# Kernel optimization log

Hardware: AMD Instinct MI355X
Metric: run time of the kernel (lower is better)

## Reference

```python
import jax, jax.numpy as jnp
import numpy as np

N_QUBITS = 12
DIM = 2 ** N_QUBITS
BATCH = 2048


def setup_inputs() -> dict:
    key = jax.random.key(0)
    k1, k2, k3 = jax.random.split(key, 3)
    inputs = jax.random.normal(k1, (BATCH, N_QUBITS), dtype=jnp.float32)
    weight = jax.random.normal(k2, (3 + 2 * N_QUBITS,), dtype=jnp.float32)
    entangle_matrix = jax.random.normal(k3, (DIM, DIM), dtype=jnp.float32)
    return {"inputs": inputs, "weight": weight, "entangle_matrix": entangle_matrix}


def _encode(ry_angles, rz_angles):
    # Encoder: state = prod over qubits of first column of (Rz*Ry) per qubit.
    ry = ry_angles / 2
    rz = rz_angles / 2
    a = jnp.cos(ry) * jnp.exp(-1j * rz)  # entry11 (row bit = 0)
    b = jnp.sin(ry) * jnp.exp(1j * rz)   # entry21 (row bit = 1)
    col2 = jnp.stack([a, b], axis=-1).astype(jnp.complex64)  # [B, n, 2]
    B, n = ry.shape
    v = jnp.ones((B, 1), dtype=jnp.complex64)
    for q in range(n):  # Kronecker fold over qubits (big-endian, matches dec2bin)
        v = (v[:, :, None] * col2[:, q][:, None, :]).reshape(B, -1)
    return v  # [B, 2^n]


def _rot_mat(w):
    # rot_mat: per-qubit Rx(w[q]) @ Rz(w[n+q]), then full Kronecker product.
    n = w.shape[0] // 2
    tx = (w[:n] / 2).astype(jnp.complex64)
    tz = (w[n:] / 2).astype(jnp.complex64)
    c, s = jnp.cos(tx), jnp.sin(tx)
    rx = jnp.stack([jnp.stack([c, -1j * s], -1),
                    jnp.stack([-1j * s, c], -1)], -2)  # [n,2,2]
    ez = jnp.exp(-1j * tz)
    zero = jnp.zeros_like(ez)
    rz = jnp.stack([jnp.stack([ez, zero], -1),
                    jnp.stack([zero, jnp.exp(1j * tz)], -1)], -2)  # [n,2,2]
    mats = jnp.einsum('qij,qjk->qik', rx, rz)
    M = mats[0]
    for q in range(1, n):
        M = jnp.kron(M, mats[q])
    return M  # [2^n, 2^n]


def _ry2(theta):
    a = theta / 2
    c, s = jnp.cos(a), jnp.sin(a)
    return jnp.stack([jnp.stack([c, -s]), jnp.stack([s, c])])  # [2,2] real


def _final_rot(th3):
    # final_rot_mat: Rz-form @ Ry-form @ Rx-form (all ry_mat_list), kron with identity.
    rot = _ry2(th3[2]) @ (_ry2(th3[1]) @ _ry2(th3[0]))
    eye = jnp.eye(DIM // 2, dtype=jnp.complex64)
    return jnp.kron(rot.astype(jnp.complex64), eye)  # [DIM, DIM]


def reference(inputs, weight, entangle_matrix):
    # initial=False branch
    ry_angles = inputs
    rz_angles = jnp.square(inputs)
    v = _encode(ry_angles, rz_angles)                 # [B, DIM] complex64
    E = entangle_matrix.astype(jnp.complex64)
    R = _rot_mat(weight[3:])
    M = E @ R @ E                                     # [DIM, DIM]
    v = v @ M.T                                       # tensordot dims ([-1],[-1])
    F = _final_rot(weight[:3])
    v = v @ F.T
    half = DIM // 2
    # vector[:, half:] = 0 then sum |.|^2  <=>  sum over first half
    return jnp.sum(jnp.square(jnp.abs(v[:, :half])), axis=-1)  # [B] float32
```

## Files before the change

kernel.cpp:

```cpp
#include <hip/hip_runtime.h>
#include <math.h>

#define QDIM 4096
#define NQ 12
#define QBATCH 2048

typedef _Float16 f16x8 __attribute__((ext_vector_type(8)));
typedef float f32x4 __attribute__((ext_vector_type(4)));
typedef int i32x4 __attribute__((ext_vector_type(4)));

__device__ __forceinline__ void gld_lds16(const void* gptr, void* ldsptr) {
    __builtin_amdgcn_global_load_lds(
        (const __attribute__((address_space(1))) void*)gptr,
        (__attribute__((address_space(3))) void*)ldsptr,
        16, 0, 0);
}

__device__ __forceinline__ int q8(float x) {
    float y = fminf(fmaxf(x, -127.f), 127.f);
    return (int)rintf(y);
}
__device__ __forceinline__ int pack4_i8(int a, int b, int c, int d) {
    return (a & 0xFF) | ((b & 0xFF) << 8) | ((c & 0xFF) << 16) | ((d & 0xFF) << 24);
}

__global__ __launch_bounds__(256) void conv_kernel(
    const float* __restrict__ E, const float* __restrict__ wgt,
    _Float16* __restrict__ Eh, signed char* __restrict__ G8)
{
    float th = 0.5f * (wgt[0] + wgt[1] + wgt[2]);
    float c0 = cosf(th), c1 = -sinf(th);
    const float qs = 127.f / 6.f;
    size_t flat = ((size_t)blockIdx.x * 256 + threadIdx.x) * 8;
    size_t n = flat >> 12;
    size_t k = flat & (QDIM - 1);
    const float* p0 = E + n * QDIM + k;
    const float* p1 = p0 + (size_t)QBATCH * QDIM;
    float4 a0 = ((const float4*)p0)[0], a1 = ((const float4*)p0)[1];
    float4 b0 = ((const float4*)p1)[0], b1 = ((const float4*)p1)[1];
    f16x8 h0 = { (_Float16)a0.x, (_Float16)a0.y, (_Float16)a0.z, (_Float16)a0.w,
                 (_Float16)a1.x, (_Float16)a1.y, (_Float16)a1.z, (_Float16)a1.w };
    f16x8 h1 = { (_Float16)b0.x, (_Float16)b0.y, (_Float16)b0.z, (_Float16)b0.w,
                 (_Float16)b1.x, (_Float16)b1.y, (_Float16)b1.z, (_Float16)b1.w };
    *(f16x8*)&Eh[n * QDIM + k] = h0;
    *(f16x8*)&Eh[(n + QBATCH) * QDIM + k] = h1;
    float g[8] = { c0*a0.x + c1*b0.x, c0*a0.y + c1*b0.y, c0*a0.z + c1*b0.z, c0*a0.w + c1*b0.w,
                   c0*a1.x + c1*b1.x, c0*a1.y + c1*b1.y, c0*a1.z + c1*b1.z, c0*a1.w + c1*b1.w };
    int2 gp = { pack4_i8(q8(g[0]*qs), q8(g[1]*qs), q8(g[2]*qs), q8(g[3]*qs)),
                pack4_i8(q8(g[4]*qs), q8(g[5]*qs), q8(g[6]*qs), q8(g[7]*qs)) };
    *(int2*)&G8[n * QDIM + k] = gp;
}

__global__ __launch_bounds__(256) void expand_kernel(
    const float* __restrict__ inputs, _Float16* __restrict__ A1)
{
    __shared__ float ab[NQ][4];
    const int b = blockIdx.x;
    const int tid = threadIdx.x;
    if (tid < NQ) {
        float x = inputs[b * NQ + tid];
        float ry = 0.5f * x;
        float rz = 0.5f * x * x;
        float ca = cosf(ry), sa = sinf(ry), cz = cosf(rz), sz = sinf(rz);
        ab[tid][0] = ca * cz;  ab[tid][1] = -ca * sz;
        ab[tid][2] = sa * cz;  ab[tid][3] =  sa * sz;
    }
    __syncthreads();
    float pr0 = 1.f, pi0 = 0.f;
#pragma unroll
    for (int q = 0; q < 8; ++q) {
        int bit = (tid >> (7 - q)) & 1;
        float cr = ab[q][bit * 2 + 0], ci = ab[q][bit * 2 + 1];
        float nr = pr0 * cr - pi0 * ci;
        float ni = pr0 * ci + pi0 * cr;
        pr0 = nr; pi0 = ni;
    }
    f16x8 vr[2], vi[2];
#pragma unroll
    for (int u = 0; u < 16; ++u) {
        float pr = pr0, pi = pi0;
#pragma unroll
        for (int q = 8; q < 12; ++q) {
            int bit = (u >> (11 - q)) & 1;
            float cr = ab[q][bit * 2 + 0], ci = ab[q][bit * 2 + 1];
            float nr = pr * cr - pi * ci;
            float ni = pr * ci + pi * cr;
            pr = nr; pi = ni;
        }
        vr[u >> 3][u & 7] = (_Float16)pr;
        vi[u >> 3][u & 7] = (_Float16)pi;
    }
    const int idx0 = tid * 16;
    *(f16x8*)&A1[(size_t)b * QDIM + idx0] = vr[0];
    *(f16x8*)&A1[(size_t)b * QDIM + idx0 + 8] = vr[1];
    *(f16x8*)&A1[(size_t)(b + QBATCH) * QDIM + idx0] = vi[0];
    *(f16x8*)&A1[(size_t)(b + QBATCH) * QDIM + idx0 + 8] = vi[1];
}

__global__ __launch_bounds__(256) void gemm_f16(
    const _Float16* __restrict__ A, const _Float16* __restrict__ B,
    _Float16* __restrict__ C, int N)
{
    const int K = QDIM;
    __shared__ __attribute__((aligned(16))) _Float16 As[128 * 64];
    __shared__ __attribute__((aligned(16))) _Float16 Bs[128 * 64];

    const int tid  = threadIdx.x;
    const int wave = tid >> 6;
    const int lane = tid & 63;
    const int bn0 = blockIdx.x * 128;
    const int bm0 = blockIdx.y * 128;
    const int wm = (wave >> 1) * 64;
    const int wn = (wave & 1) * 64;
    const int q = lane >> 4;
    const int r = lane & 15;
    const int rx = r & 7;

    f32x4 acc[4][4];
#pragma unroll
    for (int i = 0; i < 4; ++i)
#pragma unroll
        for (int j = 0; j < 4; ++j) acc[i][j] = (f32x4){0.f, 0.f, 0.f, 0.f};

    const _Float16* gA[4];
    const _Float16* gB[4];
    char* lA[4];
    char* lB[4];
#pragma unroll
    for (int n = 0; n < 4; ++n) {
        int c = n * 256 + tid;
        int row = c >> 3;
        int gcol = (c & 7) ^ (row & 7);
        gA[n] = A + (size_t)(bm0 + row) * K + gcol * 8;
        gB[n] = B + (size_t)(bn0 + row) * K + gcol * 8;
        lA[n] = (char*)As + (n * 256 + wave * 64) * 16;
        lB[n] = (char*)Bs + (n * 256 + wave * 64) * 16;
    }

    for (int kk = 0; kk < K; kk += 64) {
#pragma unroll
        for (int n = 0; n < 4; ++n) {
            gld_lds16(gA[n] + kk, lA[n]);
            gld_lds16(gB[n] + kk, lB[n]);
        }
        __syncthreads();

#pragma unroll
        for (int s = 0; s < 2; ++s) {
            f16x8 af[4], bf[4];
#pragma unroll
            for (int i = 0; i < 4; ++i) {
                int row = wm + i * 16 + r;
                af[i] = *(const f16x8*)&As[(row * 8 + ((s * 4 + q) ^ rx)) * 8];
            }
#pragma unroll
            for (int j = 0; j < 4; ++j) {
                int row = wn + j * 16 + r;
                bf[j] = *(const f16x8*)&Bs[(row * 8 + ((s * 4 + q) ^ rx)) * 8];
            }
#pragma unroll
            for (int i = 0; i < 4; ++i)
#pragma unroll
                for (int j = 0; j < 4; ++j)
                    acc[i][j] = __builtin_amdgcn_mfma_f32_16x16x32_f16(af[i], bf[j], acc[i][j], 0, 0, 0);
        }
        __syncthreads();
    }

#pragma unroll
    for (int i = 0; i < 4; ++i) {
        const int crow = bm0 + wm + i * 16 + q * 4;
#pragma unroll
        for (int rr = 0; rr < 4; ++rr)
#pragma unroll
            for (int j = 0; j < 4; ++j)
                C[(size_t)(crow + rr) * N + bn0 + wn + j * 16 + r] = (_Float16)acc[i][j][rr];
    }
}

__global__ __launch_bounds__(256) void butterfly_kernel(
    const _Float16* __restrict__ u1, const float* __restrict__ wgt,
    signed char* __restrict__ A2, float* __restrict__ scaleA)
{
    __shared__ float sRe[QDIM];
    __shared__ float sIm[QDIM];
    __shared__ float mats[NQ][8];
    __shared__ float red[8];
    const int b = blockIdx.x;
    const int tid = threadIdx.x;

    if (tid < NQ) {
        float tx = 0.5f * wgt[3 + tid];
        float tz = 0.5f * wgt[15 + tid];
        float c = cosf(tx), s = sinf(tx), cz = cosf(tz), sz = sinf(tz);
        mats[tid][0] =  c * cz;  mats[tid][1] = -c * sz;
        mats[tid][2] =  s * sz;  mats[tid][3] = -s * cz;
        mats[tid][4] = -s * sz;  mats[tid][5] = -s * cz;
        mats[tid][6] =  c * cz;  mats[tid][7] =  c * sz;
    }
    const int base = tid * 16;
    const _Float16* pRe = u1 + (size_t)b * QDIM + base;
    const _Float16* pIm = u1 + (size_t)(b + QBATCH) * QDIM + base;
    float xr[16], xi[16];
    {
        f16x8 r0 = ((const f16x8*)pRe)[0], r1 = ((const f16x8*)pRe)[1];
        f16x8 i0 = ((const f16x8*)pIm)[0], i1 = ((const f16x8*)pIm)[1];
#pragma unroll
        for (int j = 0; j < 8; ++j) {
            xr[j] = (float)r0[j]; xr[8 + j] = (float)r1[j];
            xi[j] = (float)i0[j]; xi[8 + j] = (float)i1[j];
        }
    }
    __syncthreads();

#pragma unroll
    for (int p = 0; p < 4; ++p) {
        const int qq = 11 - p;
        const float m00r = mats[qq][0], m00i = mats[qq][1];
        const float m01r = mats[qq][2], m01i = mats[qq][3];
        const float m10r = mats[qq][4], m10i = mats[qq][5];
        const float m11r = mats[qq][6], m11i = mats[qq][7];
#pragma unroll
        for (int t = 0; t < 8; ++t) {
            int i0 = ((t >> p) << (p + 1)) | (t & ((1 << p) - 1));
            int i1 = i0 | (1 << p);
            float x0r = xr[i0], x0i = xi[i0];
            float x1r = xr[i1], x1i = xi[i1];
            xr[i0] = m00r * x0r - m00i * x0i + m01r * x1r - m01i * x1i;
            xi[i0] = m00r * x0i + m00i * x0r + m01r * x1i + m01i * x1r;
            xr[i1] = m10r * x0r - m10i * x0i + m11r * x1r - m11i * x1i;
            xi[i1] = m10r * x0i + m10i * x0r + m11r * x1i + m11i * x1r;
        }
    }
#pragma unroll
    for (int j = 0; j < 16; ++j) { sRe[base + j] = xr[j]; sIm[base + j] = xi[j]; }
    __syncthreads();

    for (int p = 4; p < 12; ++p) {
        const int qq = 11 - p;
        const float m00r = mats[qq][0], m00i = mats[qq][1];
        const float m01r = mats[qq][2], m01i = mats[qq][3];
        const float m10r = mats[qq][4], m10i = mats[qq][5];
        const float m11r = mats[qq][6], m11i = mats[qq][7];
        for (int t = tid; t < QDIM / 2; t += 256) {
            int i0 = ((t >> p) << (p + 1)) | (t & ((1 << p) - 1));
            int i1 = i0 | (1 << p);
            float x0r = sRe[i0], x0i = sIm[i0];
            float x1r = sRe[i1], x1i = sIm[i1];
            sRe[i0] = m00r * x0r - m00i * x0i + m01r * x1r - m01i * x1i;
            sIm[i0] = m00r * x0i + m00i * x0r + m01r * x1i + m01i * x1r;
            sRe[i1] = m10r * x0r - m10i * x0i + m11r * x1r - m11i * x1i;
            sIm[i1] = m10r * x0i + m10i * x0r + m11r * x1i + m11i * x1r;
        }
        __syncthreads();
    }

    float mR = 0.f, mI = 0.f;
#pragma unroll
    for (int j = 0; j < 16; ++j) {
        mR = fmaxf(mR, fabsf(sRe[base + j]));
        mI = fmaxf(mI, fabsf(sIm[base + j]));
    }
#pragma unroll
    for (int off = 32; off > 0; off >>= 1) {
        mR = fmaxf(mR, __shfl_xor(mR, off, 64));
        mI = fmaxf(mI, __shfl_xor(mI, off, 64));
    }
    const int wid = tid >> 6;
    if ((tid & 63) == 0) { red[wid] = mR; red[4 + wid] = mI; }
    __syncthreads();
    mR = fmaxf(fmaxf(red[0], red[1]), fmaxf(red[2], red[3]));
    mI = fmaxf(fmaxf(red[4], red[5]), fmaxf(red[6], red[7]));
    mR = fmaxf(mR, 1e-30f);
    mI = fmaxf(mI, 1e-30f);
    if (tid == 0) {
        scaleA[b] = mR / 127.f;
        scaleA[b + QBATCH] = mI / 127.f;
    }
    const float invR = 127.f / mR, invI = 127.f / mI;
    i32x4 qr, qi;
#pragma unroll
    for (int w = 0; w < 4; ++w) {
        qr[w] = pack4_i8(q8(sRe[base + 4*w] * invR), q8(sRe[base + 4*w + 1] * invR),
                         q8(sRe[base + 4*w + 2] * invR), q8(sRe[base + 4*w + 3] * invR));
        qi[w] = pack4_i8(q8(sIm[base + 4*w] * invI), q8(sIm[base + 4*w + 1] * invI),
                         q8(sIm[base + 4*w + 2] * invI), q8(sIm[base + 4*w + 3] * invI));
    }
    *(i32x4*)&A2[(size_t)b * QDIM + base] = qr;
    *(i32x4*)&A2[(size_t)(b + QBATCH) * QDIM + base] = qi;
}

__global__ __launch_bounds__(256) void gemm2_i8(
    const signed char* __restrict__ A, const signed char* __restrict__ B,
    const float* __restrict__ scaleA, float* __restrict__ out)
{
    const int K = QDIM;
    __shared__ __attribute__((aligned(16))) signed char As[128 * 128];
    __shared__ __attribute__((aligned(16))) signed char Bs[128 * 128];

    const int tid  = threadIdx.x;
    const int wave = tid >> 6;
    const int lane = tid & 63;
    const int bn0 = blockIdx.x * 128;
    const int bm0 = blockIdx.y * 128;
    const int wm = (wave >> 1) * 64;
    const int wn = (wave & 1) * 64;
    const int q = lane >> 4;
    const int r = lane & 15;
    const int rx = r & 7;

    i32x4 acc[4][4];
#pragma unroll
    for (int i = 0; i < 4; ++i)
#pragma unroll
        for (int j = 0; j < 4; ++j) acc[i][j] = (i32x4){0, 0, 0, 0};

    const signed char* gA[4];
    const signed char* gB[4];
    char* lA[4];
    char* lB[4];
#pragma unroll
    for (int n = 0; n < 4; ++n) {
        int c = n * 256 + tid;
        int row = c >> 3;
        int gcol = (c & 7) ^ (row & 7);
        gA[n] = A + (size_t)(bm0 + row) * K + gcol * 16;
        gB[n] = B + (size_t)(bn0 + row) * K + gcol * 16;
        lA[n] = (char*)As + (n * 256 + wave * 64) * 16;
        lB[n] = (char*)Bs + (n * 256 + wave * 64) * 16;
    }

    for (int kk = 0; kk < K; kk += 128) {
#pragma unroll
        for (int n = 0; n < 4; ++n) {
            gld_lds16(gA[n] + kk, lA[n]);
            gld_lds16(gB[n] + kk, lB[n]);
        }
        __syncthreads();

#pragma unroll
        for (int s = 0; s < 2; ++s) {
            i32x4 af[4], bf[4];
#pragma unroll
            for (int i = 0; i < 4; ++i) {
                int row = wm + i * 16 + r;
                af[i] = *(const i32x4*)&As[row * 128 + (((s * 4 + q) ^ rx) * 16)];
            }
#pragma unroll
            for (int j = 0; j < 4; ++j) {
                int row = wn + j * 16 + r;
                bf[j] = *(const i32x4*)&Bs[row * 128 + (((s * 4 + q) ^ rx) * 16)];
            }
#pragma unroll
            for (int i = 0; i < 4; ++i)
#pragma unroll
                for (int j = 0; j < 4; ++j)
                    acc[i][j] = __builtin_amdgcn_mfma_i32_16x16x64_i8(af[i], bf[j], acc[i][j], 0, 0, 0);
        }
        __syncthreads();
    }

    const float dqG = 6.f / 127.f;
#pragma unroll
    for (int i = 0; i < 4; ++i) {
#pragma unroll
        for (int rr = 0; rr < 4; ++rr) {
            const int row = bm0 + wm + i * 16 + q * 4 + rr;
            const float sc = scaleA[row] * dqG;
            float v = 0.f;
#pragma unroll
            for (int j = 0; j < 4; ++j) {
                float t = sc * (float)acc[i][j][rr];
                v = fmaf(t, t, v);
            }
            v += __shfl_xor(v, 1, 64);
            v += __shfl_xor(v, 2, 64);
            v += __shfl_xor(v, 4, 64);
            v += __shfl_xor(v, 8, 64);
            if (r == 0) atomicAdd(&out[row & (QBATCH - 1)], v);
        }
    }
}

__global__ __launch_bounds__(256) void zero_out(float* __restrict__ out) {
    ((float4*)out)[blockIdx.x * 256 + threadIdx.x] = (float4){0.f, 0.f, 0.f, 0.f};
}

extern "C" void kernel_launch(void* const* d_in, const int* in_sizes, int n_in,
                              void* d_out, int out_size, void* d_ws, size_t ws_size,
                              hipStream_t stream)
{
    const float* inputs = (const float*)d_in[0];
    const float* weight = (const float*)d_in[1];
    const float* E      = (const float*)d_in[2];
    float* out = (float*)d_out;

    char* ws = (char*)d_ws;
    const size_t MB = 1024 * 1024;
    _Float16*    Eh     = (_Float16*)   (ws + 0);
    signed char* G8     = (signed char*)(ws + 32 * MB);
    _Float16*    A1     = (_Float16*)   (ws + 40 * MB);
    _Float16*    u1     = (_Float16*)   (ws + 72 * MB);
    signed char* A2     = (signed char*)(ws + 104 * MB);
    float*       scaleA = (float*)      (ws + 120 * MB);

    conv_kernel<<<(QBATCH * QDIM / 8) / 256, 256, 0, stream>>>(E, weight, Eh, G8);
    expand_kernel<<<QBATCH, 256, 0, stream>>>(inputs, A1);
    gemm_f16<<<dim3(QDIM / 128, QDIM / 128), 256, 0, stream>>>(A1, Eh, u1, QDIM);
    butterfly_kernel<<<QBATCH, 256, 0, stream>>>(u1, weight, A2, scaleA);
    zero_out<<<QBATCH / 1024, 256, 0, stream>>>(out);
    gemm2_i8<<<dim3(2048 / 128, QDIM / 128), 256, 0, stream>>>(A2, G8, scaleA, out);
}
```

Measured before the change: 336.7 us.

## Restructure butterfly as three register-resident radix-16 passes with padded LDS transposes

Replaces the eight shared-memory butterfly stages, each ending in a barrier, with three passes of four in-register stages. Data moves between passes through padded shared-memory transposes (strides 273 and 17) meant to avoid bank conflicts. This cuts LDS traffic and barriers. The zero_out launch is removed by zeroing the output inside expand_kernel. In exchange, the final int8 stores become strided single-byte writes instead of 16-byte vector stores.

```diff
diff --git a/kernel.cpp b/kernel.cpp
--- a/kernel.cpp
+++ b/kernel.cpp
@@ -52,11 +52,13 @@
 }
 
 __global__ __launch_bounds__(256) void expand_kernel(
-    const float* __restrict__ inputs, _Float16* __restrict__ A1)
+    const float* __restrict__ inputs, _Float16* __restrict__ A1,
+    float* __restrict__ out)
 {
     __shared__ float ab[NQ][4];
     const int b = blockIdx.x;
     const int tid = threadIdx.x;
+    if (tid == 0) out[b] = 0.f;
     if (tid < NQ) {
         float x = inputs[b * NQ + tid];
         float ry = 0.5f * x;
@@ -182,12 +184,14 @@
     const _Float16* __restrict__ u1, const float* __restrict__ wgt,
     signed char* __restrict__ A2, float* __restrict__ scaleA)
 {
-    __shared__ float sRe[QDIM];
-    __shared__ float sIm[QDIM];
+    __shared__ float sRe[4366];
+    __shared__ float sIm[4366];
     __shared__ float mats[NQ][8];
     __shared__ float red[8];
-    const int b = blockIdx.x;
+    const int blk = blockIdx.x;
     const int tid = threadIdx.x;
+    const int ah = tid >> 4;
+    const int al = tid & 15;
 
     if (tid < NQ) {
         float tx = 0.5f * wgt[3 + tid];
@@ -198,11 +202,11 @@
         mats[tid][4] = -s * sz;  mats[tid][5] = -s * cz;
         mats[tid][6] =  c * cz;  mats[tid][7] =  c * sz;
     }
-    const int base = tid * 16;
-    const _Float16* pRe = u1 + (size_t)b * QDIM + base;
-    const _Float16* pIm = u1 + (size_t)(b + QBATCH) * QDIM + base;
+
     float xr[16], xi[16];
     {
+        const _Float16* pRe = u1 + (size_t)blk * QDIM + tid * 16;
+        const _Float16* pIm = u1 + (size_t)(blk + QBATCH) * QDIM + tid * 16;
         f16x8 r0 = ((const f16x8*)pRe)[0], r1 = ((const f16x8*)pRe)[1];
         f16x8 i0 = ((const f16x8*)pIm)[0], i1 = ((const f16x8*)pIm)[1];
 #pragma unroll
@@ -213,53 +217,65 @@
     }
     __syncthreads();
 
-#pragma unroll
-    for (int p = 0; p < 4; ++p) {
-        const int qq = 11 - p;
-        const float m00r = mats[qq][0], m00i = mats[qq][1];
-        const float m01r = mats[qq][2], m01i = mats[qq][3];
-        const float m10r = mats[qq][4], m10i = mats[qq][5];
-        const float m11r = mats[qq][6], m11i = mats[qq][7];
-#pragma unroll
-        for (int t = 0; t < 8; ++t) {
-            int i0 = ((t >> p) << (p + 1)) | (t & ((1 << p) - 1));
-            int i1 = i0 | (1 << p);
-            float x0r = xr[i0], x0i = xi[i0];
-            float x1r = xr[i1], x1i = xi[i1];
-            xr[i0] = m00r * x0r - m00i * x0i + m01r * x1r - m01i * x1i;
-            xi[i0] = m00r * x0i + m00i * x0r + m01r * x1i + m01i * x1r;
-            xr[i1] = m10r * x0r - m10i * x0i + m11r * x1r - m11i * x1i;
-            xi[i1] = m10r * x0i + m10i * x0r + m11r * x1i + m11i * x1r;
-        }
-    }
-#pragma unroll
-    for (int j = 0; j < 16; ++j) { sRe[base + j] = xr[j]; sIm[base + j] = xi[j]; }
+#define BFLY_STAGE(arrR, arrI, K_, Q_)                                         \
+    {                                                                          \
+        const float m00r = mats[Q_][0], m00i = mats[Q_][1];                    \
+        const float m01r = mats[Q_][2], m01i = mats[Q_][3];                    \
+        const float m10r = mats[Q_][4], m10i = mats[Q_][5];                    \
+        const float m11r = mats[Q_][6], m11i = mats[Q_][7];                    \
+        _Pragma("unroll")                                                      \
+        for (int t = 0; t < 8; ++t) {                                          \
+            int i0 = ((t >> (K_)) << ((K_) + 1)) | (t & ((1 << (K_)) - 1));    \
+            int i1 = i0 | (1 << (K_));                                         \
+            float x0r = arrR[i0], x0i = arrI[i0];                              \
+            float x1r = arrR[i1], x1i = arrI[i1];                              \
+            arrR[i0] = m00r * x0r - m00i * x0i + m01r * x1r - m01i * x1i;      \
+            arrI[i0] = m00r * x0i + m00i * x0r + m01r * x1i + m01i * x1r;      \
+            arrR[i1] = m10r * x0r - m10i * x0i + m11r * x1r - m11i * x1i;      \
+            arrI[i1] = m10r * x0i + m10i * x0r + m11r * x1i + m11i * x1r;      \
+        }                                                                      \
+    }
+
+#pragma unroll
+    for (int p = 0; p < 4; ++p) BFLY_STAGE(xr, xi, p, 11 - p);
+
+#pragma unroll
+    for (int c = 0; c < 16; ++c) {
+        sRe[273 * ah + 17 * al + c] = xr[c];
+        sIm[273 * ah + 17 * al + c] = xi[c];
+    }
     __syncthreads();
 
-    for (int p = 4; p < 12; ++p) {
-        const int qq = 11 - p;
-        const float m00r = mats[qq][0], m00i = mats[qq][1];
-        const float m01r = mats[qq][2], m01i = mats[qq][3];
-        const float m10r = mats[qq][4], m10i = mats[qq][5];
-        const float m11r = mats[qq][6], m11i = mats[qq][7];
-        for (int t = tid; t < QDIM / 2; t += 256) {
-            int i0 = ((t >> p) << (p + 1)) | (t & ((1 << p) - 1));
-            int i1 = i0 | (1 << p);
-            float x0r = sRe[i0], x0i = sIm[i0];
-            float x1r = sRe[i1], x1i = sIm[i1];
-            sRe[i0] = m00r * x0r - m00i * x0i + m01r * x1r - m01i * x1i;
-            sIm[i0] = m00r * x0i + m00i * x0r + m01r * x1i + m01i * x1r;
-            sRe[i1] = m10r * x0r - m10i * x0i + m11r * x1r - m11i * x1i;
-            sIm[i1] = m10r * x0i + m10i * x0r + m11r * x1i + m11i * x1r;
-        }
-        __syncthreads();
-    }
+    float yr[16], yi[16];
+#pragma unroll
+    for (int b = 0; b < 16; ++b) {
+        yr[b] = sRe[273 * ah + 17 * b + al];
+        yi[b] = sIm[273 * ah + 17 * b + al];
+    }
+#pragma unroll
+    for (int p = 0; p < 4; ++p) BFLY_STAGE(yr, yi, p, 7 - p);
+
+#pragma unroll
+    for (int b = 0; b < 16; ++b) {
+        sRe[273 * ah + 17 * b + al] = yr[b];
+        sIm[273 * ah + 17 * b + al] = yi[b];
+    }
+    __syncthreads();
+
+    float zr[16], zi[16];
+#pragma unroll
+    for (int a = 0; a < 16; ++a) {
+        zr[a] = sRe[273 * a + 17 * ah + al];
+        zi[a] = sIm[273 * a + 17 * ah + al];
+    }
+#pragma unroll
+    for (int p = 0; p < 4; ++p) BFLY_STAGE(zr, zi, p, 3 - p);
 
     float mR = 0.f, mI = 0.f;
 #pragma unroll
     for (int j = 0; j < 16; ++j) {
-        mR = fmaxf(mR, fabsf(sRe[base + j]));
-        mI = fmaxf(mI, fabsf(sIm[base + j]));
+        mR = fmaxf(mR, fabsf(zr[j]));
+        mI = fmaxf(mI, fabsf(zi[j]));
     }
 #pragma unroll
     for (int off = 32; off > 0; off >>= 1) {
@@ -274,20 +290,19 @@
     mR = fmaxf(mR, 1e-30f);
     mI = fmaxf(mI, 1e-30f);
     if (tid == 0) {
-        scaleA[b] = mR / 127.f;
-        scaleA[b + QBATCH] = mI / 127.f;
+        scaleA[blk] = mR / 127.f;
+        scaleA[blk + QBATCH] = mI / 127.f;
     }
     const float invR = 127.f / mR, invI = 127.f / mI;
-    i32x4 qr, qi;
-#pragma unroll
-    for (int w = 0; w < 4; ++w) {
-        qr[w] = pack4_i8(q8(sRe[base + 4*w] * invR), q8(sRe[base + 4*w + 1] * invR),
-                         q8(sRe[base + 4*w + 2] * invR), q8(sRe[base + 4*w + 3] * invR));
-        qi[w] = pack4_i8(q8(sIm[base + 4*w] * invI), q8(sIm[base + 4*w + 1] * invI),
-                         q8(sIm[base + 4*w + 2] * invI), q8(sIm[base + 4*w + 3] * invI));
-    }
-    *(i32x4*)&A2[(size_t)b * QDIM + base] = qr;
-    *(i32x4*)&A2[(size_t)(b + QBATCH) * QDIM + base] = qi;
+
+    signed char* oRe = A2 + (size_t)blk * QDIM + ah * 16 + al;
+    signed char* oIm = A2 + (size_t)(blk + QBATCH) * QDIM + ah * 16 + al;
+#pragma unroll
+    for (int a = 0; a < 16; ++a) {
+        oRe[a * 256] = (signed char)q8(zr[a] * invR);
+        oIm[a * 256] = (signed char)q8(zi[a] * invI);
+    }
+#undef BFLY_STAGE
 }
 
 __global__ __launch_bounds__(256) void gemm2_i8(
@@ -382,10 +397,6 @@
     }
 }
 
-__global__ __launch_bounds__(256) void zero_out(float* __restrict__ out) {
-    ((float4*)out)[blockIdx.x * 256 + threadIdx.x] = (float4){0.f, 0.f, 0.f, 0.f};
-}
-
 extern "C" void kernel_launch(void* const* d_in, const int* in_sizes, int n_in,
                               void* d_out, int out_size, void* d_ws, size_t ws_size,
                               hipStream_t stream)
@@ -405,9 +416,8 @@
     float*       scaleA = (float*)      (ws + 120 * MB);
 
     conv_kernel<<<(QBATCH * QDIM / 8) / 256, 256, 0, stream>>>(E, weight, Eh, G8);
-    expand_kernel<<<QBATCH, 256, 0, stream>>>(inputs, A1);
+    expand_kernel<<<QBATCH, 256, 0, stream>>>(inputs, A1, out);
     gemm_f16<<<dim3(QDIM / 128, QDIM / 128), 256, 0, stream>>>(A1, Eh, u1, QDIM);
     butterfly_kernel<<<QBATCH, 256, 0, stream>>>(u1, weight, A2, scaleA);
-    zero_out<<<QBATCH / 1024, 256, 0, stream>>>(out);
     gemm2_i8<<<dim3(2048 / 128, QDIM / 128), 256, 0, stream>>>(A2, G8, scaleA, out);
 }
```

Result: faster. 321.4 us (-4.6%).
